# Kernel tuning notes

Measured on AMD Instinct MI355X. Metric: run time of the kernel, lower is better.

## Reference

```python
import jax, jax.numpy as jnp
import numpy as np

B, H, L, D = 4, 16, 8192, 64


def setup_inputs() -> dict:
    key = jax.random.key(0)
    ks = jax.random.split(key, 10)
    q = jax.random.normal(ks[0], (B, H, L, D), dtype=jnp.float32)
    k = jax.random.normal(ks[1], (B, H, L, D), dtype=jnp.float32)
    v = jax.random.normal(ks[2], (B, H, L, D), dtype=jnp.float32)
    mask = jax.random.randint(ks[3], (B, H, L), 0, 2, dtype=jnp.int32)
    s = 1.0 / np.sqrt(D)
    Wa_w = jax.random.uniform(ks[4], (D, D), jnp.float32, -s, s)  # torch Linear weight [out,in]
    Wa_b = jax.random.uniform(ks[5], (D,), jnp.float32, -s, s)
    Ua_w = jax.random.uniform(ks[6], (D, D), jnp.float32, -s, s)
    Ua_b = jax.random.uniform(ks[7], (D,), jnp.float32, -s, s)
    va_w = jax.random.uniform(ks[8], (1, D), jnp.float32, -s, s)
    va_b = jax.random.uniform(ks[9], (1,), jnp.float32, -s, s)
    return {"q": q, "k": k, "v": v, "mask": mask,
            "Wa_w": Wa_w, "Wa_b": Wa_b, "Ua_w": Ua_w, "Ua_b": Ua_b,
            "va_w": va_w, "va_b": va_b}


def reference(q, k, v, mask, Wa_w, Wa_b, Ua_w, Ua_b, va_w, va_b):
    # e1 = Wa(q), e2 = Ua(k)  (torch Linear: x @ W.T + b)
    e1 = jnp.einsum('bhld,ed->bhle', q, Wa_w) + Wa_b
    e2 = jnp.einsum('bhld,ed->bhle', k, Ua_w) + Ua_b
    t = jnp.tanh(e1 + e2)
    # va: [B,H,L,D] -> [B,H,L]
    e = jnp.einsum('bhld,d->bhl', t, va_w[0]) + va_b[0]
    e = jnp.where(mask == 0, jnp.float32(-10000.0), e)
    alpha = jax.nn.softmax(e, axis=-1)  # softmax over sequence length
    return alpha[..., None] * v
```

## Files before the change

### kernel.cpp

```cpp
#include <hip/hip_runtime.h>
#include <hip/hip_bf16.h>

#define BH   64
#define LSEQ 8192
#define DDIM 64
#define NPOS (BH * LSEQ)

typedef __attribute__((ext_vector_type(8))) short bf16x8;
typedef __attribute__((ext_vector_type(4))) float f32x4;

__device__ inline short f2bf(float f) {
    unsigned u = __builtin_bit_cast(unsigned, f);
    unsigned r = (u + 0x7FFFu + ((u >> 16) & 1u)) >> 16;
    return (short)r;
}
__device__ inline float bf2f(short s) {
    unsigned u = ((unsigned)(unsigned short)s) << 16;
    return __builtin_bit_cast(float, u);
}

__device__ inline void split8(const float* f, bf16x8& hi, bf16x8& lo) {
#pragma unroll
    for (int j = 0; j < 8; j++) {
        short h = f2bf(f[j]);
        hi[j] = h;
        lo[j] = f2bf(f[j] - bf2f(h));
    }
}

__device__ inline float tanh_fast(float x) {
    float ex = __expf(2.f * x);
    return 1.f - 2.f * __builtin_amdgcn_rcpf(ex + 1.f);
}

__global__ __launch_bounds__(256) void score_kernel(
    const float* __restrict__ q, const float* __restrict__ k,
    const float* __restrict__ Waw, const float* __restrict__ Wab,
    const float* __restrict__ Uaw, const float* __restrict__ Uab,
    const float* __restrict__ vaw, const float* __restrict__ vab_p,
    float* __restrict__ e_out)
{
    const int lane = threadIdx.x & 63;
    const int m    = lane & 15;
    const int quad = lane >> 4;
    const int wgl  = blockIdx.x * 4 + (threadIdx.x >> 6);

    bf16x8 bwa[4][2], bua[4][2];
    float bias_s[4], vav[4];
#pragma unroll
    for (int t = 0; t < 4; t++) {
        const int n = t * 16 + m;
        bias_s[t] = Wab[n] + Uab[n];
        vav[t]    = vaw[n];
#pragma unroll
        for (int s = 0; s < 2; s++) {
            const int k0 = s * 32 + quad * 8;
            const float4 wA = ((const float4*)(Waw + n * 64 + k0))[0];
            const float4 wB = ((const float4*)(Waw + n * 64 + k0))[1];
            const float4 uA = ((const float4*)(Uaw + n * 64 + k0))[0];
            const float4 uB = ((const float4*)(Uaw + n * 64 + k0))[1];
            float wf[8] = {wA.x, wA.y, wA.z, wA.w, wB.x, wB.y, wB.z, wB.w};
            float uf[8] = {uA.x, uA.y, uA.z, uA.w, uB.x, uB.y, uB.z, uB.w};
            bf16x8 wv, uv;
#pragma unroll
            for (int j = 0; j < 8; j++) { wv[j] = f2bf(wf[j]); uv[j] = f2bf(uf[j]); }
            bwa[t][s] = wv;
            bua[t][s] = uv;
        }
    }
    const float vab = vab_p[0];

#pragma unroll 1
    for (int ti = 0; ti < 4; ++ti) {
        const long tile = (long)wgl * 4 + ti;
        const long p0   = tile * 16;

        f32x4 acc[4];
#pragma unroll
        for (int t = 0; t < 4; t++) acc[t] = (f32x4){0.f, 0.f, 0.f, 0.f};

#pragma unroll
        for (int s = 0; s < 2; s++) {
            const size_t off = (size_t)(p0 + m) * 64 + s * 32 + quad * 8;
            const float4 qa = ((const float4*)(q + off))[0];
            const float4 qb = ((const float4*)(q + off))[1];
            const float4 ka = ((const float4*)(k + off))[0];
            const float4 kb = ((const float4*)(k + off))[1];
            float qf[8] = {qa.x, qa.y, qa.z, qa.w, qb.x, qb.y, qb.z, qb.w};
            float kf[8] = {ka.x, ka.y, ka.z, ka.w, kb.x, kb.y, kb.z, kb.w};
            bf16x8 qhi, qlo, khi, klo;
            split8(qf, qhi, qlo);
            split8(kf, khi, klo);
#pragma unroll
            for (int t = 0; t < 4; t++) {
                acc[t] = __builtin_amdgcn_mfma_f32_16x16x32_bf16(qhi, bwa[t][s], acc[t], 0, 0, 0);
                acc[t] = __builtin_amdgcn_mfma_f32_16x16x32_bf16(qlo, bwa[t][s], acc[t], 0, 0, 0);
                acc[t] = __builtin_amdgcn_mfma_f32_16x16x32_bf16(khi, bua[t][s], acc[t], 0, 0, 0);
                acc[t] = __builtin_amdgcn_mfma_f32_16x16x32_bf16(klo, bua[t][s], acc[t], 0, 0, 0);
            }
        }

        float c[4] = {0.f, 0.f, 0.f, 0.f};
#pragma unroll
        for (int t = 0; t < 4; t++) {
#pragma unroll
            for (int r = 0; r < 4; r++) {
                float x = acc[t][r] + bias_s[t];
                c[r] += vav[t] * tanh_fast(x);
            }
        }
#pragma unroll
        for (int r = 0; r < 4; r++) {
#pragma unroll
            for (int off2 = 1; off2 < 16; off2 <<= 1)
                c[r] += __shfl_xor(c[r], off2, 16);
        }
        if (m == 0) {
            float4 ev = make_float4(c[0] + vab, c[1] + vab, c[2] + vab, c[3] + vab);
            *((float4*)(e_out + p0 + quad * 4)) = ev;
        }
    }
}

__global__ __launch_bounds__(1024) void softmax_kernel(
    const int* __restrict__ mask, float* __restrict__ e)
{
    const int row  = blockIdx.x;
    const size_t base = (size_t)row * LSEQ;
    const int tid  = threadIdx.x;
    const int lane = tid & 63;
    const int wv   = tid >> 6;
    __shared__ float redmax[16];
    __shared__ float redsum[16];

    float4 e0 = ((const float4*)(e + base))[tid];
    float4 e1 = ((const float4*)(e + base))[1024 + tid];
    int4  m0 = ((const int4*)(mask + base))[tid];
    int4  m1 = ((const int4*)(mask + base))[1024 + tid];

    float em[8];
    em[0] = m0.x ? e0.x : -10000.f;
    em[1] = m0.y ? e0.y : -10000.f;
    em[2] = m0.z ? e0.z : -10000.f;
    em[3] = m0.w ? e0.w : -10000.f;
    em[4] = m1.x ? e1.x : -10000.f;
    em[5] = m1.y ? e1.y : -10000.f;
    em[6] = m1.z ? e1.z : -10000.f;
    em[7] = m1.w ? e1.w : -10000.f;

    float lm = em[0];
#pragma unroll
    for (int j = 1; j < 8; j++) lm = fmaxf(lm, em[j]);
#pragma unroll
    for (int off = 32; off >= 1; off >>= 1) lm = fmaxf(lm, __shfl_xor(lm, off, 64));
    if (lane == 0) redmax[wv] = lm;
    __syncthreads();
    float M = redmax[0];
#pragma unroll
    for (int i = 1; i < 16; i++) M = fmaxf(M, redmax[i]);

    float ex[8];
    float ls = 0.f;
#pragma unroll
    for (int j = 0; j < 8; j++) { ex[j] = __expf(em[j] - M); ls += ex[j]; }
#pragma unroll
    for (int off = 32; off >= 1; off >>= 1) ls += __shfl_xor(ls, off, 64);
    if (lane == 0) redsum[wv] = ls;
    __syncthreads();
    float S = 0.f;
#pragma unroll
    for (int i = 0; i < 16; i++) S += redsum[i];
    const float inv = 1.f / S;

    float4 o0 = make_float4(ex[0] * inv, ex[1] * inv, ex[2] * inv, ex[3] * inv);
    float4 o1 = make_float4(ex[4] * inv, ex[5] * inv, ex[6] * inv, ex[7] * inv);
    ((float4*)(e + base))[tid]        = o0;
    ((float4*)(e + base))[1024 + tid] = o1;
}

__global__ __launch_bounds__(256) void scale_kernel(
    const float* __restrict__ v, const float* __restrict__ alpha,
    float* __restrict__ out)
{
    const size_t i = (size_t)blockIdx.x * 256 + threadIdx.x;
    float4 vv = ((const float4*)v)[i];
    const float a = alpha[i >> 4];
    float4 o = make_float4(a * vv.x, a * vv.y, a * vv.z, a * vv.w);
    ((float4*)out)[i] = o;
}

extern "C" void kernel_launch(void* const* d_in, const int* in_sizes, int n_in,
                              void* d_out, int out_size, void* d_ws, size_t ws_size,
                              hipStream_t stream) {
    const float* q    = (const float*)d_in[0];
    const float* k    = (const float*)d_in[1];
    const float* v    = (const float*)d_in[2];
    const int*   mask = (const int*)d_in[3];
    const float* Waw  = (const float*)d_in[4];
    const float* Wab  = (const float*)d_in[5];
    const float* Uaw  = (const float*)d_in[6];
    const float* Uab  = (const float*)d_in[7];
    const float* vaw  = (const float*)d_in[8];
    const float* vab  = (const float*)d_in[9];
    float* out = (float*)d_out;

    float* e_buf = (float*)d_ws;

    score_kernel<<<2048, 256, 0, stream>>>(q, k, Waw, Wab, Uaw, Uab, vaw, vab, e_buf);
    softmax_kernel<<<BH, 1024, 0, stream>>>(mask, e_buf);
    scale_kernel<<<NPOS * DDIM / 4 / 256, 256, 0, stream>>>(v, e_buf, out);
}
```

Before: 427.2 us.

## Double-buffer score loads, fold mask into scoring, defer softmax normalization to scale

The score kernel now issues the q/k/mask loads for the next tile before computing the current one, using two register buffers, so global loads overlap MFMA work. The mask is applied in the score kernel instead of the softmax kernel. The softmax kernel now computes only the per-row max and the inverse sum, and the scale kernel recomputes exp(e-M)*inv per element, each thread handling two float4s. This removes the write-back of normalized alpha and the mask read in the softmax pass, at the cost of extra exp work and higher register pressure in the score kernel.

```diff
diff --git a/kernel.cpp b/kernel.cpp
--- a/kernel.cpp
+++ b/kernel.cpp
@@ -5,6 +5,7 @@
 #define LSEQ 8192
 #define DDIM 64
 #define NPOS (BH * LSEQ)
+#define NT4  (NPOS * DDIM / 4)
 
 typedef __attribute__((ext_vector_type(8))) short bf16x8;
 typedef __attribute__((ext_vector_type(4))) float f32x4;
@@ -18,7 +19,6 @@
     unsigned u = ((unsigned)(unsigned short)s) << 16;
     return __builtin_bit_cast(float, u);
 }
-
 __device__ inline void split8(const float* f, bf16x8& hi, bf16x8& lo) {
 #pragma unroll
     for (int j = 0; j < 8; j++) {
@@ -27,7 +27,6 @@
         lo[j] = f2bf(f[j] - bf2f(h));
     }
 }
-
 __device__ inline float tanh_fast(float x) {
     float ex = __expf(2.f * x);
     return 1.f - 2.f * __builtin_amdgcn_rcpf(ex + 1.f);
@@ -35,6 +34,7 @@
 
 __global__ __launch_bounds__(256) void score_kernel(
     const float* __restrict__ q, const float* __restrict__ k,
+    const int*   __restrict__ mask,
     const float* __restrict__ Waw, const float* __restrict__ Wab,
     const float* __restrict__ Uaw, const float* __restrict__ Uab,
     const float* __restrict__ vaw, const float* __restrict__ vab_p,
@@ -44,6 +44,7 @@
     const int m    = lane & 15;
     const int quad = lane >> 4;
     const int wgl  = blockIdx.x * 4 + (threadIdx.x >> 6);
+    const long t0  = (long)wgl * 4;
 
     bf16x8 bwa[4][2], bua[4][2];
     float bias_s[4], vav[4];
@@ -70,22 +71,30 @@
     }
     const float vab = vab_p[0];
 
-#pragma unroll 1
-    for (int ti = 0; ti < 4; ++ti) {
-        const long tile = (long)wgl * 4 + ti;
-        const long p0   = tile * 16;
-
+    float4 A[8], B[8];
+    int4 mkA, mkB;
+
+    auto issue = [&](float4 (&buf)[8], int4& mk, long tile) {
+        mk = ((const int4*)mask)[tile * 4 + quad];
+        const size_t off = (size_t)(tile * 16 + m) * 64 + quad * 8;
+        buf[0] = *((const float4*)(q + off));
+        buf[1] = *((const float4*)(q + off + 4));
+        buf[2] = *((const float4*)(k + off));
+        buf[3] = *((const float4*)(k + off + 4));
+        buf[4] = *((const float4*)(q + off + 32));
+        buf[5] = *((const float4*)(q + off + 36));
+        buf[6] = *((const float4*)(k + off + 32));
+        buf[7] = *((const float4*)(k + off + 36));
+    };
+
+    auto compute = [&](const float4 (&buf)[8], const int4& mk, long tile) {
         f32x4 acc[4];
 #pragma unroll
         for (int t = 0; t < 4; t++) acc[t] = (f32x4){0.f, 0.f, 0.f, 0.f};
-
 #pragma unroll
         for (int s = 0; s < 2; s++) {
-            const size_t off = (size_t)(p0 + m) * 64 + s * 32 + quad * 8;
-            const float4 qa = ((const float4*)(q + off))[0];
-            const float4 qb = ((const float4*)(q + off))[1];
-            const float4 ka = ((const float4*)(k + off))[0];
-            const float4 kb = ((const float4*)(k + off))[1];
+            const float4 qa = buf[s * 4 + 0], qb = buf[s * 4 + 1];
+            const float4 ka = buf[s * 4 + 2], kb = buf[s * 4 + 3];
             float qf[8] = {qa.x, qa.y, qa.z, qa.w, qb.x, qb.y, qb.z, qb.w};
             float kf[8] = {ka.x, ka.y, ka.z, ka.w, kb.x, kb.y, kb.z, kb.w};
             bf16x8 qhi, qlo, khi, klo;
@@ -99,15 +108,12 @@
                 acc[t] = __builtin_amdgcn_mfma_f32_16x16x32_bf16(klo, bua[t][s], acc[t], 0, 0, 0);
             }
         }
-
         float c[4] = {0.f, 0.f, 0.f, 0.f};
 #pragma unroll
         for (int t = 0; t < 4; t++) {
 #pragma unroll
-            for (int r = 0; r < 4; r++) {
-                float x = acc[t][r] + bias_s[t];
-                c[r] += vav[t] * tanh_fast(x);
-            }
+            for (int r = 0; r < 4; r++)
+                c[r] += vav[t] * tanh_fast(acc[t][r] + bias_s[t]);
         }
 #pragma unroll
         for (int r = 0; r < 4; r++) {
@@ -116,16 +122,29 @@
                 c[r] += __shfl_xor(c[r], off2, 16);
         }
         if (m == 0) {
-            float4 ev = make_float4(c[0] + vab, c[1] + vab, c[2] + vab, c[3] + vab);
-            *((float4*)(e_out + p0 + quad * 4)) = ev;
-        }
-    }
-}
-
-__global__ __launch_bounds__(1024) void softmax_kernel(
-    const int* __restrict__ mask, float* __restrict__ e)
+            float4 ev;
+            ev.x = mk.x ? c[0] + vab : -10000.f;
+            ev.y = mk.y ? c[1] + vab : -10000.f;
+            ev.z = mk.z ? c[2] + vab : -10000.f;
+            ev.w = mk.w ? c[3] + vab : -10000.f;
+            *((float4*)(e_out + tile * 16 + quad * 4)) = ev;
+        }
+    };
+
+    issue(A, mkA, t0 + 0);
+    issue(B, mkB, t0 + 1);
+    compute(A, mkA, t0 + 0);
+    issue(A, mkA, t0 + 2);
+    compute(B, mkB, t0 + 1);
+    issue(B, mkB, t0 + 3);
+    compute(A, mkA, t0 + 2);
+    compute(B, mkB, t0 + 3);
+}
+
+__global__ __launch_bounds__(1024) void rowstat_kernel(
+    const float* __restrict__ e, float* __restrict__ stats)
 {
-    const int row  = blockIdx.x;
+    const int row = blockIdx.x;
     const size_t base = (size_t)row * LSEQ;
     const int tid  = threadIdx.x;
     const int lane = tid & 63;
@@ -135,18 +154,7 @@
 
     float4 e0 = ((const float4*)(e + base))[tid];
     float4 e1 = ((const float4*)(e + base))[1024 + tid];
-    int4  m0 = ((const int4*)(mask + base))[tid];
-    int4  m1 = ((const int4*)(mask + base))[1024 + tid];
-
-    float em[8];
-    em[0] = m0.x ? e0.x : -10000.f;
-    em[1] = m0.y ? e0.y : -10000.f;
-    em[2] = m0.z ? e0.z : -10000.f;
-    em[3] = m0.w ? e0.w : -10000.f;
-    em[4] = m1.x ? e1.x : -10000.f;
-    em[5] = m1.y ? e1.y : -10000.f;
-    em[6] = m1.z ? e1.z : -10000.f;
-    em[7] = m1.w ? e1.w : -10000.f;
+    float em[8] = {e0.x, e0.y, e0.z, e0.w, e1.x, e1.y, e1.z, e1.w};
 
     float lm = em[0];
 #pragma unroll
@@ -159,34 +167,43 @@
 #pragma unroll
     for (int i = 1; i < 16; i++) M = fmaxf(M, redmax[i]);
 
-    float ex[8];
     float ls = 0.f;
 #pragma unroll
-    for (int j = 0; j < 8; j++) { ex[j] = __expf(em[j] - M); ls += ex[j]; }
+    for (int j = 0; j < 8; j++) ls += __expf(em[j] - M);
 #pragma unroll
     for (int off = 32; off >= 1; off >>= 1) ls += __shfl_xor(ls, off, 64);
     if (lane == 0) redsum[wv] = ls;
     __syncthreads();
-    float S = 0.f;
-#pragma unroll
-    for (int i = 0; i < 16; i++) S += redsum[i];
-    const float inv = 1.f / S;
-
-    float4 o0 = make_float4(ex[0] * inv, ex[1] * inv, ex[2] * inv, ex[3] * inv);
-    float4 o1 = make_float4(ex[4] * inv, ex[5] * inv, ex[6] * inv, ex[7] * inv);
-    ((float4*)(e + base))[tid]        = o0;
-    ((float4*)(e + base))[1024 + tid] = o1;
+    if (tid == 0) {
+        float S = 0.f;
+#pragma unroll
+        for (int i = 0; i < 16; i++) S += redsum[i];
+        stats[row * 2]     = M;
+        stats[row * 2 + 1] = 1.f / S;
+    }
 }
 
 __global__ __launch_bounds__(256) void scale_kernel(
-    const float* __restrict__ v, const float* __restrict__ alpha,
-    float* __restrict__ out)
+    const float* __restrict__ v, const float* __restrict__ e,
+    const float* __restrict__ stats, float* __restrict__ out)
 {
-    const size_t i = (size_t)blockIdx.x * 256 + threadIdx.x;
-    float4 vv = ((const float4*)v)[i];
-    const float a = alpha[i >> 4];
-    float4 o = make_float4(a * vv.x, a * vv.y, a * vv.z, a * vv.w);
-    ((float4*)out)[i] = o;
+    const size_t i0 = (size_t)blockIdx.x * 256 + threadIdx.x;
+    const size_t i1 = i0 + (size_t)(NT4 / 2);
+
+    float4 v0 = ((const float4*)v)[i0];
+    float4 v1 = ((const float4*)v)[i1];
+    const size_t p0 = i0 >> 4, p1 = i1 >> 4;
+    float e0 = e[p0], e1 = e[p1];
+    const size_t r0 = p0 >> 13, r1 = p1 >> 13;
+    float M0 = stats[r0 * 2], I0 = stats[r0 * 2 + 1];
+    float M1 = stats[r1 * 2], I1 = stats[r1 * 2 + 1];
+
+    float a0 = __expf(e0 - M0) * I0;
+    float a1 = __expf(e1 - M1) * I1;
+    float4 o0 = make_float4(a0 * v0.x, a0 * v0.y, a0 * v0.z, a0 * v0.w);
+    float4 o1 = make_float4(a1 * v1.x, a1 * v1.y, a1 * v1.z, a1 * v1.w);
+    ((float4*)out)[i0] = o0;
+    ((float4*)out)[i1] = o1;
 }
 
 extern "C" void kernel_launch(void* const* d_in, const int* in_sizes, int n_in,
@@ -205,8 +222,9 @@
     float* out = (float*)d_out;
 
     float* e_buf = (float*)d_ws;
-
-    score_kernel<<<2048, 256, 0, stream>>>(q, k, Waw, Wab, Uaw, Uab, vaw, vab, e_buf);
-    softmax_kernel<<<BH, 1024, 0, stream>>>(mask, e_buf);
-    scale_kernel<<<NPOS * DDIM / 4 / 256, 256, 0, stream>>>(v, e_buf, out);
-}
+    float* stats = (float*)d_ws + NPOS;
+
+    score_kernel<<<2048, 256, 0, stream>>>(q, k, mask, Waw, Wab, Uaw, Uab, vaw, vab, e_buf);
+    rowstat_kernel<<<BH, 1024, 0, stream>>>(e_buf, stats);
+    scale_kernel<<<NT4 / 2 / 256, 256, 0, stream>>>(v, e_buf, stats, out);
+}
```

After: 418.5 us. 1.02x faster.
